# Kernel optimization log

Hardware: AMD Instinct MI355X
Metric: run time of the kernel (lower is better)

## Reference

```python
import jax, jax.numpy as jnp
import numpy as np

TEMPERATURE = 0.1
NUM_CLASSES = 100


def setup_inputs() -> dict:
    key = jax.random.key(0)
    k1, k2 = jax.random.split(key)
    embeddings = jax.random.normal(k1, (8192, 128), dtype=jnp.float32)
    labels = jax.random.randint(k2, (8192,), 0, NUM_CLASSES, dtype=jnp.int64)
    return {"embeddings": embeddings, "labels": labels}


def reference(embeddings, labels):
    # L2-normalize rows (eps matches torch.nn.functional.normalize clamp)
    norm = jnp.maximum(jnp.linalg.norm(embeddings, axis=1, keepdims=True), 1e-12)
    e = embeddings / norm
    sim = jnp.matmul(e, e.T) / TEMPERATURE  # [N, N]
    n = sim.shape[0]
    eye = jnp.eye(n, dtype=bool)
    # positives: same label, excluding self
    pos = (labels[None, :] == labels[:, None]) & ~eye
    # The per-row torch loop computes soft-target cross-entropy over all
    # non-diagonal entries: row_loss_i = -sum_{j in pos(i)} log_softmax(sim[i, j!=i])_j.
    # log_softmax is permutation-invariant, so concatenation order is irrelevant.
    neg_inf = jnp.finfo(sim.dtype).min
    masked = jnp.where(eye, neg_inf, sim)
    logz = jax.nn.logsumexp(masked, axis=1, keepdims=True)  # [N, 1]
    logp = sim - logz  # [N, N]
    row_loss = -jnp.sum(jnp.where(pos, logp, 0.0), axis=1)  # rows with no positives contribute 0
    return jnp.sum(row_loss) / n
```

## Files before the change

kernel.cpp:

```cpp
#include <hip/hip_runtime.h>


#define N 8192
#define D 128
#define NCLS 100
#define NTILE 512
#define RLCAP 256
#define MWIN 8
#define YGRID 32
#define XGRID 36
#define LDS_TILES 20
#define SQK 3.79828256f
#define LN2 0.69314718055994530942f

typedef __bf16 bf16x8 __attribute__((ext_vector_type(8)));
typedef float f32x4 __attribute__((ext_vector_type(4)));

#define EBF_OFF  0x000000u
#define ENORM_OFF 0x200000u
#define CNT_OFF  0x600000u
#define Z_OFF    0x600200u
#define RL_OFF   0x608200u
#define S_OFF    0x621200u
#define ZERO_SZ  (512u + 32768u)

__device__ __forceinline__ unsigned short f32_to_bf16_rne(float f) {
    unsigned int u = __float_as_uint(f);
    u += 0x7fffu + ((u >> 16) & 1u);
    return (unsigned short)(u >> 16);
}


__global__ __launch_bounds__(256) void prep_kernel(
        const float* __restrict__ emb, const int* __restrict__ labels,
        unsigned char* __restrict__ ebf, int* __restrict__ cnt,
        float* __restrict__ enorm, int* __restrict__ rowlist) {
    const int w    = threadIdx.x >> 6;
    const int lane = threadIdx.x & 63;
    const int h    = lane >> 5;
    const int li   = lane & 31;
    const int row  = blockIdx.x * 8 + w * 2 + h;

    const float4 v = *(const float4*)(emb + (size_t)row * D + li * 4);
    float ss = v.x * v.x + v.y * v.y + v.z * v.z + v.w * v.w;
    #pragma unroll
    for (int off = 16; off; off >>= 1) ss += __shfl_xor(ss, off);
    const float inv = 1.0f / fmaxf(sqrtf(ss), 1e-12f);
    const float e0 = v.x * inv, e1 = v.y * inv, e2 = v.z * inv, e3 = v.w * inv;

    const int grp = row >> 4, col = row & 15;
    const int c = li >> 3, q = (li >> 1) & 3, jh = li & 1;
    uint2 packed;
    packed.x = (unsigned)f32_to_bf16_rne(e0 * SQK) | ((unsigned)f32_to_bf16_rne(e1 * SQK) << 16);
    packed.y = (unsigned)f32_to_bf16_rne(e2 * SQK) | ((unsigned)f32_to_bf16_rne(e3 * SQK) << 16);
    *(uint2*)(ebf + grp * 4096 + c * 1024 + q * 256 + col * 16 + jh * 8) = packed;

    *(float4*)(enorm + (size_t)row * D + li * 4) = make_float4(e0, e1, e2, e3);

    if (li == 0) {
        const int lab = labels[row];
        int slot = atomicAdd(&cnt[lab], 1);
        slot = slot < RLCAP ? slot : RLCAP - 1;
        rowlist[lab * RLCAP + slot] = row;
    }
}

__global__ __launch_bounds__(256) void zsum_kernel(
        const unsigned char* __restrict__ ebf, float* __restrict__ z,
        const float* __restrict__ enorm, const int* __restrict__ cnt,
        const int* __restrict__ rowlist, float* __restrict__ S) {
    const int t = threadIdx.x;

    if (blockIdx.x >= 32) {
        const int eidx = (blockIdx.x - 32) * YGRID + blockIdx.y;
        if (eidx >= NCLS || t >= 128) return;
        const int d = t;
        const int n = cnt[eidx] < RLCAP ? cnt[eidx] : RLCAP;
        const int* rl = rowlist + eidx * RLCAP;
        float acc = 0.0f;
        int idx = 0;
        for (; idx + 4 <= n; idx += 4) {
            const int r0 = rl[idx], r1 = rl[idx + 1], r2 = rl[idx + 2], r3 = rl[idx + 3];
            acc += enorm[(size_t)r0 * D + d] + enorm[(size_t)r1 * D + d]
                 + enorm[(size_t)r2 * D + d] + enorm[(size_t)r3 * D + d];
        }
        for (; idx < n; ++idx)
            acc += enorm[(size_t)rl[idx] * D + d];
        S[eidx * D + d] = acc;
        return;
    }

    __shared__ float zcol[LDS_TILES * 16];
    const int w    = t >> 6;
    const int lane = t & 63;
    const int q    = lane >> 4;
    const int col  = lane & 15;
    const int bi   = blockIdx.x;
    const int y    = blockIdx.y;
    const int ti0  = bi * 16 + w * 4;
    const int m_lo = y * MWIN + 1;
    const bool lowhalf = (bi < 16);

    for (int e = t; e < LDS_TILES * 16; e += 256) zcol[e] = 0.0f;

    bf16x8 a[4][4];
    #pragma unroll
    for (int g = 0; g < 4; ++g) {
        const unsigned char* ag = ebf + (size_t)(ti0 + g) * 4096 + lane * 16;
        #pragma unroll
        for (int c = 0; c < 4; ++c) a[g][c] = *(const bf16x8*)(ag + c * 1024);
    }

    f32x4 zacc4[4] = {{0.f,0.f,0.f,0.f},{0.f,0.f,0.f,0.f},
                      {0.f,0.f,0.f,0.f},{0.f,0.f,0.f,0.f}};

    __syncthreads();

    if (y == 0) {
        #pragma unroll
        for (int g = 0; g < 4; ++g) {
            const unsigned char* bg = ebf + (size_t)(ti0 + g) * 4096 + lane * 16;
            bf16x8 bd[4];
            #pragma unroll
            for (int c = 0; c < 4; ++c) bd[c] = *(const bf16x8*)(bg + c * 1024);
            f32x4 acc = {0.f, 0.f, 0.f, 0.f};
            #pragma unroll
            for (int c = 0; c < 4; ++c)
                acc = __builtin_amdgcn_mfma_f32_16x16x32_bf16(a[g][c], bd[c], acc, 0, 0, 0);
            #pragma unroll
            for (int r = 0; r < 4; ++r)
                zacc4[g][r] += (col == q * 4 + r) ? 0.0f
                    : __builtin_amdgcn_exp2f(acc[r]);
        }
    }

    const int ns = MWIN + ((y == 29 || y == 30 || (y == 31 && lowhalf)) ? 1 : 0);
    const int m_x = 228 + y;

    const int rot = 2 * w;

    bf16x8 bc[4];
    {
        const int m0 = m_lo + (rot & (MWIN - 1));
        const int tj = (ti0 + m0) & (NTILE - 1);
        const unsigned char* bg = ebf + (size_t)tj * 4096 + lane * 16;
        #pragma unroll
        for (int c = 0; c < 4; ++c) bc[c] = *(const bf16x8*)(bg + c * 1024);
    }

    #pragma unroll 2
    for (int s = 0; s < ns; ++s) {
        const int m = (s < MWIN) ? (m_lo + ((s + rot) & (MWIN - 1))) : m_x;

        const int sn = (s + 1 < ns) ? s + 1 : s;
        const int mn = (sn < MWIN) ? (m_lo + ((sn + rot) & (MWIN - 1))) : m_x;
        bf16x8 bn[4];
        {
            const int tjn = (ti0 + mn) & (NTILE - 1);
            const unsigned char* bg = ebf + (size_t)tjn * 4096 + lane * 16;
            #pragma unroll
            for (int c = 0; c < 4; ++c) bn[c] = *(const bf16x8*)(bg + c * 1024);
        }

        f32x4 ct = {0.f, 0.f, 0.f, 0.f};
        #pragma unroll
        for (int g = 0; g < 4; ++g) {
            const int d = m - g;
            const bool act = (d >= 1 && d <= 255) || (d == 256 && lowhalf);
            if (act) {
                f32x4 acc = {0.f, 0.f, 0.f, 0.f};
                __builtin_amdgcn_s_setprio(1);
                #pragma unroll
                for (int c = 0; c < 4; ++c)
                    acc = __builtin_amdgcn_mfma_f32_16x16x32_bf16(a[g][c], bc[c], acc, 0, 0, 0);
                __builtin_amdgcn_s_setprio(0);
                f32x4 p;
                #pragma unroll
                for (int r = 0; r < 4; ++r)
                    p[r] = __builtin_amdgcn_exp2f(acc[r]);
                zacc4[g] += p;
                ct += p;
            }
        }

        float ctot = (ct[0] + ct[1]) + (ct[2] + ct[3]);
        ctot += __shfl_xor(ctot, 16);
        ctot += __shfl_xor(ctot, 32);
        if (q == 0 && ctot != 0.0f) {
            if (s < MWIN) {
                const int rel = w * 4 + (m - m_lo);
                atomicAdd(&zcol[rel * 16 + col], ctot);
            } else {
                const int tj = (ti0 + m) & (NTILE - 1);
                atomicAdd(&z[tj * 16 + col], ctot);
            }
        }

        #pragma unroll
        for (int c = 0; c < 4; ++c) bc[c] = bn[c];
    }

    #pragma unroll
    for (int g = 0; g < 4; ++g)
        #pragma unroll
        for (int r = 0; r < 4; ++r) {
            float zv = zacc4[g][r];
            zv += __shfl_xor(zv, 1);
            zv += __shfl_xor(zv, 2);
            zv += __shfl_xor(zv, 4);
            zv += __shfl_xor(zv, 8);
            if (col == 0)
                atomicAdd(&z[(ti0 + g) * 16 + q * 4 + r], zv);
        }

    __syncthreads();
    for (int e = t; e < LDS_TILES * 16; e += 256) {
        const float v = zcol[e];
        if (v != 0.0f) {
            const int tj = (bi * 16 + m_lo + (e >> 4)) & (NTILE - 1);
            atomicAdd(&z[tj * 16 + (e & 15)], v);
        }
    }
}

__global__ __launch_bounds__(1024) void final_kernel(
        const int* __restrict__ labels, const int* __restrict__ cnt,
        const float* __restrict__ z, const float* __restrict__ S,
        float* __restrict__ out) {
    __shared__ float part[16];
    const int tid = threadIdx.x;
    float acc = 0.0f;
    #pragma unroll
    for (int k = 0; k < N / 1024; ++k) {
        const int row = k * 1024 + tid;
        const int P = cnt[labels[row]] - 1;
        if (P > 0)
            acc += (float)P * (LN2 * __builtin_amdgcn_logf(z[row]));
    }
    #pragma unroll
    for (int k = 0; k < (NCLS * D + 1023) / 1024; ++k) {
        const int idx = k * 1024 + tid;
        if (idx < NCLS * D) {
            const float sv = S[idx];
            acc -= 10.0f * sv * sv;
        }
    }
    #pragma unroll
    for (int off = 32; off; off >>= 1) acc += __shfl_xor(acc, off);
    if ((tid & 63) == 0) part[tid >> 6] = acc;
    __syncthreads();
    if (tid == 0) {
        float tot = 0.0f;
        #pragma unroll
        for (int w = 0; w < 16; ++w) tot += part[w];
        out[0] = (tot + 10.0f * (float)N) * (1.0f / (float)N);
    }
}

extern "C" void kernel_launch(void* const* d_in, const int* in_sizes, int n_in,
                              void* d_out, int out_size, void* d_ws, size_t ws_size,
                              hipStream_t stream) {
    const float* emb  = (const float*)d_in[0];
    const int* labels = (const int*)d_in[1];
    float* out        = (float*)d_out;
    char* ws          = (char*)d_ws;

    unsigned char* ebf = (unsigned char*)(ws + EBF_OFF);
    float* enorm       = (float*)(ws + ENORM_OFF);
    int*   cnt         = (int*)(ws + CNT_OFF);
    float* z           = (float*)(ws + Z_OFF);
    int*   rowlist     = (int*)(ws + RL_OFF);
    float* S           = (float*)(ws + S_OFF);

    hipMemsetAsync(ws + CNT_OFF, 0, ZERO_SZ, stream);

    prep_kernel<<<N / 8, 256, 0, stream>>>(emb, labels, ebf, cnt, enorm, rowlist);
    zsum_kernel<<<dim3(XGRID, YGRID), 256, 0, stream>>>(ebf, z, enorm, cnt, rowlist, S);
    final_kernel<<<1, 1024, 0, stream>>>(labels, cnt, z, S, out);
}
```

Baseline: 125.1 us.

## Fuse final reduction into zsum via last-block counter and shrink memset

Removes the separate final_kernel launch. The last block to finish zsum_kernel, detected with an atomic counter and threadfence, now does the log/S reduction and writes the output. The z array is zeroed inside prep_kernel, so the memset shrinks to the count region. The per-wave rotation of the column-tile order is also dropped, which may change how L2 accesses are spread. The cost is one serial tail reduction done by a single 256-thread block instead of 1024 threads, plus a global atomic per block.

```diff
diff --git a/kernel.cpp b/kernel.cpp
--- a/kernel.cpp
+++ b/kernel.cpp
@@ -9,6 +9,7 @@
 #define MWIN 8
 #define YGRID 32
 #define XGRID 36
+#define NBLK (XGRID * YGRID)
 #define LDS_TILES 20
 #define SQK 3.79828256f
 #define LN2 0.69314718055994530942f
@@ -22,7 +23,8 @@
 #define Z_OFF    0x600200u
 #define RL_OFF   0x608200u
 #define S_OFF    0x621200u
-#define ZERO_SZ  (512u + 32768u)
+#define ZERO_SZ  512u
+#define CTR_SLOT 120
 
 __device__ __forceinline__ unsigned short f32_to_bf16_rne(float f) {
     unsigned int u = __float_as_uint(f);
@@ -34,12 +36,15 @@
 __global__ __launch_bounds__(256) void prep_kernel(
         const float* __restrict__ emb, const int* __restrict__ labels,
         unsigned char* __restrict__ ebf, int* __restrict__ cnt,
-        float* __restrict__ enorm, int* __restrict__ rowlist) {
+        float* __restrict__ enorm, int* __restrict__ rowlist,
+        float* __restrict__ z) {
     const int w    = threadIdx.x >> 6;
     const int lane = threadIdx.x & 63;
     const int h    = lane >> 5;
     const int li   = lane & 31;
     const int row  = blockIdx.x * 8 + w * 2 + h;
+
+    if (threadIdx.x < 8) z[blockIdx.x * 8 + threadIdx.x] = 0.0f;
 
     const float4 v = *(const float4*)(emb + (size_t)row * D + li * 4);
     float ss = v.x * v.x + v.y * v.y + v.z * v.z + v.w * v.w;
@@ -67,193 +72,186 @@
 
 __global__ __launch_bounds__(256) void zsum_kernel(
         const unsigned char* __restrict__ ebf, float* __restrict__ z,
-        const float* __restrict__ enorm, const int* __restrict__ cnt,
-        const int* __restrict__ rowlist, float* __restrict__ S) {
+        const float* __restrict__ enorm, int* __restrict__ cnt,
+        const int* __restrict__ rowlist, float* __restrict__ S,
+        const int* __restrict__ labels, float* __restrict__ out) {
+    __shared__ float zcol[LDS_TILES * 16];
+    __shared__ float part[4];
+    __shared__ unsigned lastflag;
     const int t = threadIdx.x;
 
     if (blockIdx.x >= 32) {
         const int eidx = (blockIdx.x - 32) * YGRID + blockIdx.y;
-        if (eidx >= NCLS || t >= 128) return;
-        const int d = t;
-        const int n = cnt[eidx] < RLCAP ? cnt[eidx] : RLCAP;
-        const int* rl = rowlist + eidx * RLCAP;
-        float acc = 0.0f;
-        int idx = 0;
-        for (; idx + 4 <= n; idx += 4) {
-            const int r0 = rl[idx], r1 = rl[idx + 1], r2 = rl[idx + 2], r3 = rl[idx + 3];
-            acc += enorm[(size_t)r0 * D + d] + enorm[(size_t)r1 * D + d]
-                 + enorm[(size_t)r2 * D + d] + enorm[(size_t)r3 * D + d];
-        }
-        for (; idx < n; ++idx)
-            acc += enorm[(size_t)rl[idx] * D + d];
-        S[eidx * D + d] = acc;
-        return;
-    }
-
-    __shared__ float zcol[LDS_TILES * 16];
-    const int w    = t >> 6;
-    const int lane = t & 63;
-    const int q    = lane >> 4;
-    const int col  = lane & 15;
-    const int bi   = blockIdx.x;
-    const int y    = blockIdx.y;
-    const int ti0  = bi * 16 + w * 4;
-    const int m_lo = y * MWIN + 1;
-    const bool lowhalf = (bi < 16);
-
-    for (int e = t; e < LDS_TILES * 16; e += 256) zcol[e] = 0.0f;
-
-    bf16x8 a[4][4];
-    #pragma unroll
-    for (int g = 0; g < 4; ++g) {
-        const unsigned char* ag = ebf + (size_t)(ti0 + g) * 4096 + lane * 16;
-        #pragma unroll
-        for (int c = 0; c < 4; ++c) a[g][c] = *(const bf16x8*)(ag + c * 1024);
-    }
-
-    f32x4 zacc4[4] = {{0.f,0.f,0.f,0.f},{0.f,0.f,0.f,0.f},
-                      {0.f,0.f,0.f,0.f},{0.f,0.f,0.f,0.f}};
-
-    __syncthreads();
-
-    if (y == 0) {
+        if (eidx < NCLS && t < 128) {
+            const int d = t;
+            const int n = cnt[eidx] < RLCAP ? cnt[eidx] : RLCAP;
+            const int* rl = rowlist + eidx * RLCAP;
+            float acc = 0.0f;
+            int idx = 0;
+            for (; idx + 4 <= n; idx += 4) {
+                const int r0 = rl[idx], r1 = rl[idx + 1], r2 = rl[idx + 2], r3 = rl[idx + 3];
+                acc += enorm[(size_t)r0 * D + d] + enorm[(size_t)r1 * D + d]
+                     + enorm[(size_t)r2 * D + d] + enorm[(size_t)r3 * D + d];
+            }
+            for (; idx < n; ++idx)
+                acc += enorm[(size_t)rl[idx] * D + d];
+            S[eidx * D + d] = acc;
+        }
+    } else {
+        const int w    = t >> 6;
+        const int lane = t & 63;
+        const int q    = lane >> 4;
+        const int col  = lane & 15;
+        const int bi   = blockIdx.x;
+        const int y    = blockIdx.y;
+        const int ti0  = bi * 16 + w * 4;
+        const int m_lo = y * MWIN + 1;
+        const bool lowhalf = (bi < 16);
+
+        for (int e = t; e < LDS_TILES * 16; e += 256) zcol[e] = 0.0f;
+
+        bf16x8 a[4][4];
         #pragma unroll
         for (int g = 0; g < 4; ++g) {
-            const unsigned char* bg = ebf + (size_t)(ti0 + g) * 4096 + lane * 16;
-            bf16x8 bd[4];
-            #pragma unroll
-            for (int c = 0; c < 4; ++c) bd[c] = *(const bf16x8*)(bg + c * 1024);
-            f32x4 acc = {0.f, 0.f, 0.f, 0.f};
-            #pragma unroll
-            for (int c = 0; c < 4; ++c)
-                acc = __builtin_amdgcn_mfma_f32_16x16x32_bf16(a[g][c], bd[c], acc, 0, 0, 0);
-            #pragma unroll
-            for (int r = 0; r < 4; ++r)
-                zacc4[g][r] += (col == q * 4 + r) ? 0.0f
-                    : __builtin_amdgcn_exp2f(acc[r]);
+            const unsigned char* ag = ebf + (size_t)(ti0 + g) * 4096 + lane * 16;
+            #pragma unroll
+            for (int c = 0; c < 4; ++c) a[g][c] = *(const bf16x8*)(ag + c * 1024);
+        }
+
+        f32x4 zacc4[4] = {{0.f,0.f,0.f,0.f},{0.f,0.f,0.f,0.f},
+                          {0.f,0.f,0.f,0.f},{0.f,0.f,0.f,0.f}};
+
+        __syncthreads();
+
+        if (y == 0) {
+            #pragma unroll
+            for (int g = 0; g < 4; ++g) {
+                const unsigned char* bg = ebf + (size_t)(ti0 + g) * 4096 + lane * 16;
+                bf16x8 bd[4];
+                #pragma unroll
+                for (int c = 0; c < 4; ++c) bd[c] = *(const bf16x8*)(bg + c * 1024);
+                f32x4 acc = {0.f, 0.f, 0.f, 0.f};
+                #pragma unroll
+                for (int c = 0; c < 4; ++c)
+                    acc = __builtin_amdgcn_mfma_f32_16x16x32_bf16(a[g][c], bd[c], acc, 0, 0, 0);
+                #pragma unroll
+                for (int r = 0; r < 4; ++r)
+                    zacc4[g][r] += (col == q * 4 + r) ? 0.0f
+                        : __builtin_amdgcn_exp2f(acc[r]);
+            }
+        }
+
+        const int ns = MWIN + ((y == 29 || y == 30 || (y == 31 && lowhalf)) ? 1 : 0);
+        const int m_x = 228 + y;
+
+        bf16x8 bc[4];
+        {
+            const int tj = (ti0 + m_lo) & (NTILE - 1);
+            const unsigned char* bg = ebf + (size_t)tj * 4096 + lane * 16;
+            #pragma unroll
+            for (int c = 0; c < 4; ++c) bc[c] = *(const bf16x8*)(bg + c * 1024);
+        }
+
+        #pragma unroll 2
+        for (int s = 0; s < ns; ++s) {
+            const int m = (s < MWIN) ? (m_lo + s) : m_x;
+
+            const int sn = (s + 1 < ns) ? s + 1 : s;
+            const int mn = (sn < MWIN) ? (m_lo + sn) : m_x;
+            bf16x8 bn[4];
+            {
+                const int tjn = (ti0 + mn) & (NTILE - 1);
+                const unsigned char* bg = ebf + (size_t)tjn * 4096 + lane * 16;
+                #pragma unroll
+                for (int c = 0; c < 4; ++c) bn[c] = *(const bf16x8*)(bg + c * 1024);
+            }
+
+            f32x4 ct = {0.f, 0.f, 0.f, 0.f};
+            #pragma unroll
+            for (int g = 0; g < 4; ++g) {
+                const int d = m - g;
+                const bool act = (d >= 1 && d <= 255) || (d == 256 && lowhalf);
+                if (act) {
+                    f32x4 acc = {0.f, 0.f, 0.f, 0.f};
+                    __builtin_amdgcn_s_setprio(1);
+                    #pragma unroll
+                    for (int c = 0; c < 4; ++c)
+                        acc = __builtin_amdgcn_mfma_f32_16x16x32_bf16(a[g][c], bc[c], acc, 0, 0, 0);
+                    __builtin_amdgcn_s_setprio(0);
+                    f32x4 p;
+                    #pragma unroll
+                    for (int r = 0; r < 4; ++r)
+                        p[r] = __builtin_amdgcn_exp2f(acc[r]);
+                    zacc4[g] += p;
+                    ct += p;
+                }
+            }
+
+            float ctot = (ct[0] + ct[1]) + (ct[2] + ct[3]);
+            ctot += __shfl_xor(ctot, 16);
+            ctot += __shfl_xor(ctot, 32);
+            if (q == 0 && ctot != 0.0f) {
+                if (s < MWIN) {
+                    const int rel = w * 4 + (m - m_lo);
+                    atomicAdd(&zcol[rel * 16 + col], ctot);
+                } else {
+                    const int tj = (ti0 + m) & (NTILE - 1);
+                    atomicAdd(&z[tj * 16 + col], ctot);
+                }
+            }
+
+            #pragma unroll
+            for (int c = 0; c < 4; ++c) bc[c] = bn[c];
+        }
+
+        #pragma unroll
+        for (int g = 0; g < 4; ++g)
+            #pragma unroll
+            for (int r = 0; r < 4; ++r) {
+                float zv = zacc4[g][r];
+                zv += __shfl_xor(zv, 1);
+                zv += __shfl_xor(zv, 2);
+                zv += __shfl_xor(zv, 4);
+                zv += __shfl_xor(zv, 8);
+                if (col == 0)
+                    atomicAdd(&z[(ti0 + g) * 16 + q * 4 + r], zv);
+            }
+
+        __syncthreads();
+        for (int e = t; e < LDS_TILES * 16; e += 256) {
+            const float v = zcol[e];
+            if (v != 0.0f) {
+                const int tj = (bi * 16 + m_lo + (e >> 4)) & (NTILE - 1);
+                atomicAdd(&z[tj * 16 + (e & 15)], v);
+            }
         }
     }
 
-    const int ns = MWIN + ((y == 29 || y == 30 || (y == 31 && lowhalf)) ? 1 : 0);
-    const int m_x = 228 + y;
-
-    const int rot = 2 * w;
-
-    bf16x8 bc[4];
-    {
-        const int m0 = m_lo + (rot & (MWIN - 1));
-        const int tj = (ti0 + m0) & (NTILE - 1);
-        const unsigned char* bg = ebf + (size_t)tj * 4096 + lane * 16;
+    __threadfence();
+    __syncthreads();
+    if (t == 0) lastflag = atomicAdd((unsigned*)&cnt[CTR_SLOT], 1u);
+    __syncthreads();
+    if (lastflag == NBLK - 1) {
+        __threadfence();
+        float acc = 0.0f;
+        #pragma unroll 4
+        for (int k = 0; k < N / 256; ++k) {
+            const int row = k * 256 + t;
+            const int P = cnt[labels[row]] - 1;
+            if (P > 0)
+                acc += (float)P * (LN2 * __builtin_amdgcn_logf(z[row]));
+        }
+        for (int k = t; k < NCLS * D; k += 256) {
+            const float sv = S[k];
+            acc -= 10.0f * sv * sv;
+        }
         #pragma unroll
-        for (int c = 0; c < 4; ++c) bc[c] = *(const bf16x8*)(bg + c * 1024);
-    }
-
-    #pragma unroll 2
-    for (int s = 0; s < ns; ++s) {
-        const int m = (s < MWIN) ? (m_lo + ((s + rot) & (MWIN - 1))) : m_x;
-
-        const int sn = (s + 1 < ns) ? s + 1 : s;
-        const int mn = (sn < MWIN) ? (m_lo + ((sn + rot) & (MWIN - 1))) : m_x;
-        bf16x8 bn[4];
-        {
-            const int tjn = (ti0 + mn) & (NTILE - 1);
-            const unsigned char* bg = ebf + (size_t)tjn * 4096 + lane * 16;
-            #pragma unroll
-            for (int c = 0; c < 4; ++c) bn[c] = *(const bf16x8*)(bg + c * 1024);
-        }
-
-        f32x4 ct = {0.f, 0.f, 0.f, 0.f};
-        #pragma unroll
-        for (int g = 0; g < 4; ++g) {
-            const int d = m - g;
-            const bool act = (d >= 1 && d <= 255) || (d == 256 && lowhalf);
-            if (act) {
-                f32x4 acc = {0.f, 0.f, 0.f, 0.f};
-                __builtin_amdgcn_s_setprio(1);
-                #pragma unroll
-                for (int c = 0; c < 4; ++c)
-                    acc = __builtin_amdgcn_mfma_f32_16x16x32_bf16(a[g][c], bc[c], acc, 0, 0, 0);
-                __builtin_amdgcn_s_setprio(0);
-                f32x4 p;
-                #pragma unroll
-                for (int r = 0; r < 4; ++r)
-                    p[r] = __builtin_amdgcn_exp2f(acc[r]);
-                zacc4[g] += p;
-                ct += p;
-            }
-        }
-
-        float ctot = (ct[0] + ct[1]) + (ct[2] + ct[3]);
-        ctot += __shfl_xor(ctot, 16);
-        ctot += __shfl_xor(ctot, 32);
-        if (q == 0 && ctot != 0.0f) {
-            if (s < MWIN) {
-                const int rel = w * 4 + (m - m_lo);
-                atomicAdd(&zcol[rel * 16 + col], ctot);
-            } else {
-                const int tj = (ti0 + m) & (NTILE - 1);
-                atomicAdd(&z[tj * 16 + col], ctot);
-            }
-        }
-
-        #pragma unroll
-        for (int c = 0; c < 4; ++c) bc[c] = bn[c];
-    }
-
-    #pragma unroll
-    for (int g = 0; g < 4; ++g)
-        #pragma unroll
-        for (int r = 0; r < 4; ++r) {
-            float zv = zacc4[g][r];
-            zv += __shfl_xor(zv, 1);
-            zv += __shfl_xor(zv, 2);
-            zv += __shfl_xor(zv, 4);
-            zv += __shfl_xor(zv, 8);
-            if (col == 0)
-                atomicAdd(&z[(ti0 + g) * 16 + q * 4 + r], zv);
-        }
-
-    __syncthreads();
-    for (int e = t; e < LDS_TILES * 16; e += 256) {
-        const float v = zcol[e];
-        if (v != 0.0f) {
-            const int tj = (bi * 16 + m_lo + (e >> 4)) & (NTILE - 1);
-            atomicAdd(&z[tj * 16 + (e & 15)], v);
-        }
-    }
-}
-
-__global__ __launch_bounds__(1024) void final_kernel(
-        const int* __restrict__ labels, const int* __restrict__ cnt,
-        const float* __restrict__ z, const float* __restrict__ S,
-        float* __restrict__ out) {
-    __shared__ float part[16];
-    const int tid = threadIdx.x;
-    float acc = 0.0f;
-    #pragma unroll
-    for (int k = 0; k < N / 1024; ++k) {
-        const int row = k * 1024 + tid;
-        const int P = cnt[labels[row]] - 1;
-        if (P > 0)
-            acc += (float)P * (LN2 * __builtin_amdgcn_logf(z[row]));
-    }
-    #pragma unroll
-    for (int k = 0; k < (NCLS * D + 1023) / 1024; ++k) {
-        const int idx = k * 1024 + tid;
-        if (idx < NCLS * D) {
-            const float sv = S[idx];
-            acc -= 10.0f * sv * sv;
-        }
-    }
-    #pragma unroll
-    for (int off = 32; off; off >>= 1) acc += __shfl_xor(acc, off);
-    if ((tid & 63) == 0) part[tid >> 6] = acc;
-    __syncthreads();
-    if (tid == 0) {
-        float tot = 0.0f;
-        #pragma unroll
-        for (int w = 0; w < 16; ++w) tot += part[w];
-        out[0] = (tot + 10.0f * (float)N) * (1.0f / (float)N);
+        for (int off = 32; off; off >>= 1) acc += __shfl_xor(acc, off);
+        if ((t & 63) == 0) part[t >> 6] = acc;
+        __syncthreads();
+        if (t == 0)
+            out[0] = ((part[0] + part[1]) + (part[2] + part[3]) + 10.0f * (float)N)
+                     * (1.0f / (float)N);
     }
 }
 
@@ -274,7 +272,7 @@
 
     hipMemsetAsync(ws + CNT_OFF, 0, ZERO_SZ, stream);
 
-    prep_kernel<<<N / 8, 256, 0, stream>>>(emb, labels, ebf, cnt, enorm, rowlist);
-    zsum_kernel<<<dim3(XGRID, YGRID), 256, 0, stream>>>(ebf, z, enorm, cnt, rowlist, S);
-    final_kernel<<<1, 1024, 0, stream>>>(labels, cnt, z, S, out);
-}
+    prep_kernel<<<N / 8, 256, 0, stream>>>(emb, labels, ebf, cnt, enorm, rowlist, z);
+    zsum_kernel<<<dim3(XGRID, YGRID), 256, 0, stream>>>(ebf, z, enorm, cnt, rowlist, S,
+                                                        labels, out);
+}
```

Measured after the change: 208.3 us. 1.67x slower.
